# Kernel optimization log

Measured on AMD Instinct MI355X. Metric: run time of the kernel, lower is better.

Reference implementation:

```python
import jax, jax.numpy as jnp
import numpy as np

N = 50000   # nodes
E = 300000  # directed edges
IN = 512
H = 256
OUT = 256
K = 4096    # K_target; since K < N, pooled node count Kc == K statically


def setup_inputs() -> dict:
    key = jax.random.key(0)
    ks = jax.random.split(key, 8)
    x = jax.random.normal(ks[0], (N, IN), jnp.float32)
    edge_index = jax.random.randint(ks[1], (2, E), 0, N)
    W1 = jax.random.normal(ks[2], (IN, H), jnp.float32) / np.float32(np.sqrt(IN))
    b1 = jnp.zeros((H,), jnp.float32)
    W2 = jax.random.normal(ks[3], (H, OUT), jnp.float32) / np.float32(np.sqrt(H))
    b2 = jnp.zeros((OUT,), jnp.float32)
    w_score = jax.random.normal(ks[4], (H,), jnp.float32) / np.float32(np.sqrt(H))
    W_skip = jax.random.normal(ks[5], (H, OUT), jnp.float32) / np.float32(np.sqrt(H))
    b_skip = jnp.zeros((OUT,), jnp.float32)
    return dict(x=x, edge_index=edge_index, W1=W1, b1=b1, W2=W2, b2=b2,
                w_score=w_score, W_skip=W_skip, b_skip=b_skip)


def _gcn_sparse(x, src, dst, W, b, n):
    # PyG GCNConv(add_self_loops=True, normalize=True): out = D^{-1/2}(A+I)D^{-1/2} x W + b,
    # degrees computed on dst after adding self loops.
    h = x @ W
    loop = jnp.arange(n)
    s = jnp.concatenate([src, loop])
    d = jnp.concatenate([dst, loop])
    deg = jax.ops.segment_sum(jnp.ones_like(d, h.dtype), d, num_segments=n)
    dinv = jnp.where(deg > 0, jax.lax.rsqrt(deg), 0.0)
    coef = (dinv[s] * dinv[d])[:, None]
    return jax.ops.segment_sum(h[s] * coef, d, num_segments=n) + b


def _forward(x, edge_index, W1, b1, W2, b2, w_score, W_skip, b_skip):
    n = x.shape[0]
    src, dst = edge_index[0], edge_index[1]

    # conv1 + relu (dropout is identity in eval mode)
    x1 = jax.nn.relu(_gcn_sparse(x, src, dst, W1, b1, n))
    raw = x1 @ w_score                       # [N] score (Linear, no bias)
    x1g = x1 * jnp.tanh(raw)[:, None]        # gated features

    # top-K node selection
    _, kept = jax.lax.top_k(raw, K)          # sorted descending, like torch.topk
    keep_mask = jnp.zeros((n,), bool).at[kept].set(True)
    deg = jax.ops.segment_sum(jnp.ones((src.shape[0],), jnp.int32), src, num_segments=n)

    # cluster ids: kept nodes get 0..K-1 in topk order
    cid = jnp.full((n,), -1, jnp.int32).at[kept].set(jnp.arange(K, dtype=jnp.int32))

    # non-kept nodes join the kept (undirected) neighbor with max degree;
    # encode (degree, -node_id) so segment_max picks max degree, tie-break smallest id
    s_all = jnp.concatenate([src, dst])
    t_all = jnp.concatenate([dst, src])
    cand = jnp.where(keep_mask[t_all], deg[t_all] * n + (n - 1 - t_all), -1)
    best = jax.ops.segment_max(cand, s_all, num_segments=n)  # empty segs -> int min
    has = best >= 0
    best_t = (n - 1) - jnp.where(has, best % n, 0)
    # global fallback: kept node with max degree (tie-break: earliest in topk order)
    enc_k = deg[kept] * K + (K - 1 - jnp.arange(K))
    bg = kept[jnp.argmax(enc_k)]
    cid = jnp.where(keep_mask, cid, jnp.where(has, cid[best_t], cid[bg]))

    # mean pooling per cluster (pool_by_partition)
    sums = jax.ops.segment_sum(x1g, cid, num_segments=K)
    cnt = jnp.maximum(jax.ops.segment_sum(jnp.ones((n,), x.dtype), cid, num_segments=K), 1.0)
    xp = sums / cnt[:, None]

    # pooled edges with dedup + self-pair removal, as dense KxK adjacency (rows = dst)
    cu, cv = cid[src], cid[dst]
    A = jnp.zeros((K, K), x.dtype).at[cv, cu].max((cu != cv).astype(x.dtype))
    Ahat = A + jnp.eye(K, dtype=x.dtype)
    di = jax.lax.rsqrt(Ahat.sum(axis=1))     # deg >= 1 from self loops
    An = di[:, None] * Ahat * di[None, :]

    # conv2 on pooled graph, broadcast back, skip connection
    xp2 = An @ (xp @ W2) + b2
    return xp2[cid] + x1 @ W_skip + b_skip


def reference(x, edge_index, W1, b1, W2, b2, w_score, W_skip, b_skip):
    return _forward(x, edge_index, W1, b1, W2, b2, w_score, W_skip, b_skip)
```

## Files before the change

### kernel.cpp

```cpp
#include <hip/hip_runtime.h>
#include <hip/hip_bf16.h>

#define N_NODES 50000
#define E_EDGES 300000
#define IN_F 512
#define H_F 256
#define OUT_F 256
#define K_CL 4096
#define KW (K_CL / 32)
#define PCH 128
#define THRESH 192
#define MAXH 1024
#define NSPL 32
#define NB2 ((N_NODES + 255) / 256)
#define KBW ((N_NODES + 63) / 64 + 8)

typedef short bh8 __attribute__((ext_vector_type(8)));
typedef float f4 __attribute__((ext_vector_type(4)));
typedef unsigned short u16;
typedef unsigned long long u64;

__device__ __forceinline__ unsigned fkey(float f) {
    unsigned u = __float_as_uint(f);
    return (u & 0x80000000u) ? ~u : (u | 0x80000000u);
}

__device__ __forceinline__ u16 f2bf(float f) {
    __hip_bfloat16 b = __float2bfloat16(f);
    return *reinterpret_cast<u16*>(&b);
}

__device__ __forceinline__ float bf2f(u16 u) {
    return __uint_as_float(((unsigned)u) << 16);
}

__device__ __forceinline__ int getbit(const u64* __restrict__ bits, int i) {
    return (int)((bits[i >> 6] >> (i & 63)) & 1ULL);
}

__global__ __launch_bounds__(256) void init_nodes(int* cntD, int* degS,
                                                  unsigned long long* best_enc,
                                                  int* bgnode, int* heavycnt,
                                                  unsigned long long* bestpack,
                                                  unsigned* selT, int* curk, int* hist4) {
    int i = blockIdx.x * blockDim.x + threadIdx.x;
    if (i < N_NODES) { cntD[i] = 0; degS[i] = 0; best_enc[i] = 0ULL; }
    if (i < 1024) hist4[i] = 0;
    if (i == 0) {
        *heavycnt = 0; *bgnode = 0x7FFFFFFF; *bestpack = 0ULL;
        *selT = 0u; *curk = K_CL;
    }
}

__global__ __launch_bounds__(256) void deg_edges(const int* __restrict__ src,
                                                 const int* __restrict__ dst,
                                                 int* cntD, int* degS) {
    int e = blockIdx.x * blockDim.x + threadIdx.x;
    if (e >= E_EDGES) return;
    atomicAdd(&cntD[dst[e]], 1);
    atomicAdd(&degS[src[e]], 1);
}

#define SBM 64
#define SBN 128
#define SBK 16
__global__ __launch_bounds__(256) void gemm_f32s(const float* __restrict__ A,
                                                 const float* __restrict__ B,
                                                 float* __restrict__ C,
                                                 int M, int Nc, int Kd) {
    __shared__ float As[2][SBM][SBK];
    __shared__ float Bs[2][SBK][SBN];
    int tid = threadIdx.x;
    int tx = tid & 15;
    int ty = tid >> 4;
    int lane = tid & 63;
    int wave = tid >> 6;
    int row0 = blockIdx.y * SBM, col0 = blockIdx.x * SBN;
    float acc[4][8] = {};

    int arow = wave * 16 + (lane >> 2);
    int acolf = ((((lane & 3) * 16) ^ (((lane >> 4) & 1) << 5)) >> 2);

    auto stage_B = [&](int k0, int bb) {
        #pragma unroll
        for (int u = 0; u < 2; ++u) {
            int chunk = wave * 2 + u;
            int krow = chunk * 2 + (lane >> 5);
            const float* gsrc = &B[(long)(k0 + krow) * Nc + col0 + (lane & 31) * 4];
            __builtin_amdgcn_global_load_lds(
                (const __attribute__((address_space(1))) void*)gsrc,
                (__attribute__((address_space(3))) void*)&Bs[bb][chunk * 2][0],
                16, 0, 0);
        }
    };
    auto stage_A = [&](int k0, int bb) {
        int gr = row0 + arow;
        if (gr > M - 1) gr = M - 1;
        const float* gsrc = &A[(long)gr * Kd + k0 + acolf];
        __builtin_amdgcn_global_load_lds(
            (const __attribute__((address_space(1))) void*)gsrc,
            (__attribute__((address_space(3))) void*)&As[bb][wave * 16][0],
            16, 0, 0);
    };
    auto compute = [&](int bb) {
        #pragma unroll
        for (int kq = 0; kq < 4; ++kq) {
            float4 af[4];
            #pragma unroll
            for (int i = 0; i < 4; ++i) {
                int row = ty * 4 + i;
                int cb = ((kq * 16 ^ (((row >> 2) & 1) << 5)) >> 2);
                af[i] = *(const float4*)&As[bb][row][cb];
            }
            #pragma unroll
            for (int kk = 0; kk < 4; ++kk) {
                int k = kq * 4 + kk;
                float4 b0 = *(const float4*)&Bs[bb][k][tx * 4];
                float4 b1 = *(const float4*)&Bs[bb][k][tx * 4 + 64];
                float bv[8] = {b0.x, b0.y, b0.z, b0.w, b1.x, b1.y, b1.z, b1.w};
                float av[4] = {af[0][kk], af[1][kk], af[2][kk], af[3][kk]};
                #pragma unroll
                for (int i = 0; i < 4; ++i)
                    #pragma unroll
                    for (int j = 0; j < 8; ++j)
                        acc[i][j] += av[i] * bv[j];
            }
        }
    };

    stage_B(0, 0);
    stage_A(0, 0);
    __syncthreads();
    int nt = Kd / SBK;
    for (int t = 0; t < nt; ++t) {
        int cb = t & 1;
        if (t + 1 < nt) {
            stage_B(SBK * (t + 1), cb ^ 1);
            stage_A(SBK * (t + 1), cb ^ 1);
        }
        compute(cb);
        __syncthreads();
    }

    #pragma unroll
    for (int i = 0; i < 4; ++i) {
        int gr = row0 + ty * 4 + i;
        if (gr >= M) continue;
        float4 o0 = {acc[i][0], acc[i][1], acc[i][2], acc[i][3]};
        float4 o1 = {acc[i][4], acc[i][5], acc[i][6], acc[i][7]};
        *(float4*)&C[(long)gr * Nc + col0 + tx * 4] = o0;
        *(float4*)&C[(long)gr * Nc + col0 + 64 + tx * 4] = o1;
    }
}

__global__ __launch_bounds__(256) void pack_W2(const float* __restrict__ Wa, u16* Bpa,
                                               const float* __restrict__ Wb, u16* Bpb) {
    int k = blockIdx.x & 255;
    const float* W = (blockIdx.x < 256) ? Wa : Wb;
    u16* Bp = (blockIdx.x < 256) ? Bpa : Bpb;
    int col = threadIdx.x;
    int kb = k >> 5, g = (k >> 3) & 3, j = k & 7;
    Bp[(((long)(kb * 4 + g) * 256) + col) * 8 + j] = f2bf(W[(long)k * 256 + col]);
}

__global__ __launch_bounds__(256) void gemm_mfma(const u16* __restrict__ Ab,
                                                 const float* __restrict__ Af32,
                                                 const int* __restrict__ cnt,
                                                 const u16* __restrict__ Bp,
                                                 float* __restrict__ C,
                                                 int M,
                                                 const int* __restrict__ cid,
                                                 const float* __restrict__ xp2,
                                                 const float* __restrict__ bskip) {
    int tid = threadIdx.x;
    int w = tid >> 6, l = tid & 63;
    int lo16 = l & 15, hi4 = l >> 4;
    int arow = blockIdx.x * 64 + w * 16 + lo16;
    f4 acc[16];
    #pragma unroll
    for (int n = 0; n < 16; ++n) acc[n] = (f4){0.f, 0.f, 0.f, 0.f};

    float s = 1.f;
    if (Af32 && arow < M) s = 1.f / fmaxf((float)cnt[arow], 1.f);

    #pragma unroll
    for (int kb = 0; kb < 8; ++kb) {
        bh8 a = {0, 0, 0, 0, 0, 0, 0, 0};
        if (arow < M) {
            if (Af32) {
                float4 v0 = *(const float4*)&Af32[(long)arow * 256 + kb * 32 + hi4 * 8];
                float4 v1 = *(const float4*)&Af32[(long)arow * 256 + kb * 32 + hi4 * 8 + 4];
                u16 tmp[8] = {f2bf(v0.x * s), f2bf(v0.y * s), f2bf(v0.z * s), f2bf(v0.w * s),
                              f2bf(v1.x * s), f2bf(v1.y * s), f2bf(v1.z * s), f2bf(v1.w * s)};
                a = *(const bh8*)tmp;
            } else {
                a = *(const bh8*)&Ab[(long)arow * 256 + kb * 32 + hi4 * 8];
            }
        }
        const u16* bbase = &Bp[(((long)(kb * 4 + hi4)) * 256 + lo16) * 8];
        #pragma unroll
        for (int n = 0; n < 16; ++n) {
            bh8 b = *(const bh8*)&bbase[(long)n * 128];
            acc[n] = __builtin_amdgcn_mfma_f32_16x16x32_bf16(a, b, acc[n], 0, 0, 0);
        }
    }

    int orow0 = blockIdx.x * 64 + w * 16 + hi4 * 4;
    #pragma unroll
    for (int r = 0; r < 4; ++r) {
        int gr = orow0 + r;
        if (gr >= M) continue;
        long rb = (long)gr * 256;
        const float* xrow = cid ? (xp2 + (long)cid[gr] * 256) : nullptr;
        #pragma unroll
        for (int n = 0; n < 16; ++n) {
            int gc = n * 16 + lo16;
            float v = acc[n][r];
            if (cid) v += xrow[gc] + bskip[gc];
            C[rb + gc] = v;
        }
    }
}

__global__ __launch_bounds__(256) void scan_l1(const int* __restrict__ cnt,
                                               int* bsum, int n, float* dinv) {
    __shared__ int s[256];
    int t = threadIdx.x;
    int i = blockIdx.x * 256 + t;
    int v = (i < n) ? cnt[i] : 0;
    if (dinv && i < n) dinv[i] = rsqrtf((float)v + 1.0f);
    s[t] = v;
    __syncthreads();
    for (int off = 128; off > 0; off >>= 1) {
        if (t < off) s[t] += s[t + off];
        __syncthreads();
    }
    if (t == 0) bsum[blockIdx.x] = s[0];
}

__global__ __launch_bounds__(256) void scan_l2(const int* __restrict__ bsum,
                                               int* bstart, int nb) {
    __shared__ int s[256];
    int t = threadIdx.x;
    int v = (t < nb) ? bsum[t] : 0;
    s[t] = v;
    __syncthreads();
    for (int off = 1; off < 256; off <<= 1) {
        int a = (t >= off) ? s[t - off] : 0;
        __syncthreads();
        s[t] += a;
        __syncthreads();
    }
    if (t < nb) bstart[t] = s[t] - v;
}

__global__ __launch_bounds__(256) void scan_l3(const int* __restrict__ cnt,
                                               const int* __restrict__ bstart,
                                               int* start, int* cur, int n) {
    __shared__ int s[256];
    int t = threadIdx.x;
    int i = blockIdx.x * 256 + t;
    int v = (i < n) ? cnt[i] : 0;
    s[t] = v;
    __syncthreads();
    for (int off = 1; off < 256; off <<= 1) {
        int a = (t >= off) ? s[t - off] : 0;
        __syncthreads();
        s[t] += a;
        __syncthreads();
    }
    int st = bstart[blockIdx.x] + s[t] - v;
    if (i < n) { start[i] = st; cur[i] = st; }
    if (i == n - 1) start[n] = st + v;
}

__global__ __launch_bounds__(256) void csr_scatter(const int* __restrict__ src,
                                                   const int* __restrict__ dst,
                                                   int* cur, int* csr) {
    int e = blockIdx.x * blockDim.x + threadIdx.x;
    if (e >= E_EDGES) return;
    int d = dst[e];
    int p = atomicAdd(&cur[d], 1);
    csr[p] = src[e];
}

__global__ __launch_bounds__(64) void agg_fused(const float* __restrict__ h,
                                                const float* __restrict__ dinv,
                                                const int* __restrict__ rowptr,
                                                const int* __restrict__ csr,
                                                const float* __restrict__ b1,
                                                const float* __restrict__ w_score,
                                                u16* __restrict__ x1b,
                                                float* __restrict__ raw) {
    int i = blockIdx.x;
    int l = threadIdx.x;
    float di_ = dinv[i];
    const float4* H4 = (const float4*)h;
    long q = (long)i * 64 + l;
    float4 a = H4[q];
    float sc = di_ * di_;
    a.x *= sc; a.y *= sc; a.z *= sc; a.w *= sc;
    int p0 = rowptr[i], p1 = rowptr[i + 1];
    int t = p0;
    for (; t + 1 < p1; t += 2) {
        int s0 = csr[t], s1 = csr[t + 1];
        float c0 = dinv[s0] * di_;
        float c1 = dinv[s1] * di_;
        float4 h0 = H4[(long)s0 * 64 + l];
        float4 h1 = H4[(long)s1 * 64 + l];
        a.x += c0 * h0.x; a.y += c0 * h0.y; a.z += c0 * h0.z; a.w += c0 * h0.w;
        a.x += c1 * h1.x; a.y += c1 * h1.y; a.z += c1 * h1.z; a.w += c1 * h1.w;
    }
    if (t < p1) {
        int s0 = csr[t];
        float c0 = dinv[s0] * di_;
        float4 h0 = H4[(long)s0 * 64 + l];
        a.x += c0 * h0.x; a.y += c0 * h0.y; a.z += c0 * h0.z; a.w += c0 * h0.w;
    }
    float4 bb = ((const float4*)b1)[l];
    float v0 = fmaxf(a.x + bb.x, 0.f);
    float v1 = fmaxf(a.y + bb.y, 0.f);
    float v2 = fmaxf(a.z + bb.z, 0.f);
    float v3 = fmaxf(a.w + bb.w, 0.f);
    ushort4 o;
    o.x = f2bf(v0); o.y = f2bf(v1); o.z = f2bf(v2); o.w = f2bf(v3);
    ((ushort4*)x1b)[q] = o;
    float4 wv = ((const float4*)w_score)[l];
    float s2 = (v0 * wv.x + v2 * wv.z) + (v1 * wv.y + v3 * wv.w);
    #pragma unroll
    for (int off = 32; off > 0; off >>= 1)
        s2 += __shfl_xor(s2, off, 64);
    if (l == 0) raw[i] = s2;
}

__global__ __launch_bounds__(256) void radix_hist(const float* __restrict__ raw,
                                                  const unsigned* __restrict__ pPrefix,
                                                  int byte, int* hist) {
    __shared__ int lh[256];
    int t = threadIdx.x;
    lh[t] = 0;
    __syncthreads();
    int i = blockIdx.x * 256 + t;
    if (i < N_NODES) {
        unsigned key = fkey(raw[i]);
        unsigned known_mask = (byte == 3) ? 0u : (0xFFFFFFFFu << ((byte + 1) * 8));
        if ((key & known_mask) == *pPrefix)
            atomicAdd(&lh[(key >> (byte * 8)) & 255], 1);
    }
    __syncthreads();
    int hh = lh[t];
    if (hh) atomicAdd(&hist[t], hh);
}

__global__ __launch_bounds__(64) void radix_pick(const int* __restrict__ hist,
                                                 unsigned* pPrefix, int* pK, int byte) {
    if (threadIdx.x != 0) return;
    int kk = *pK;
    int cum = 0;
    int v = 255;
    for (; v > 0; --v) {
        int c = hist[v];
        if (cum + c >= kk) break;
        cum += c;
    }
    *pPrefix |= ((unsigned)v) << (byte * 8);
    *pK = kk - cum;
}

__global__ __launch_bounds__(256) void topk_count(const float* __restrict__ raw,
                                                  const unsigned* pT,
                                                  int* bGt, int* bEq) {
    __shared__ int sg[256], se[256];
    unsigned T = *pT;
    int t = threadIdx.x;
    int i = blockIdx.x * 256 + t;
    int gt = 0, eq = 0;
    if (i < N_NODES) {
        unsigned k = fkey(raw[i]);
        gt = k > T; eq = (k == T);
    }
    sg[t] = gt; se[t] = eq;
    __syncthreads();
    for (int off = 128; off > 0; off >>= 1) {
        if (t < off) { sg[t] += sg[t + off]; se[t] += se[t + off]; }
        __syncthreads();
    }
    if (t == 0) { bGt[blockIdx.x] = sg[0]; bEq[blockIdx.x] = se[0]; }
}

__global__ __launch_bounds__(256) void scan_blocks(const int* __restrict__ bGt,
                                                   const int* __restrict__ bEq,
                                                   int* gtStart, int* eqStart) {
    __shared__ int sg[256], se[256];
    int t = threadIdx.x;
    int vg = (t < NB2) ? bGt[t] : 0;
    int ve = (t < NB2) ? bEq[t] : 0;
    sg[t] = vg; se[t] = ve;
    __syncthreads();
    for (int off = 1; off < 256; off <<= 1) {
        int a = (t >= off) ? sg[t - off] : 0;
        int b = (t >= off) ? se[t - off] : 0;
        __syncthreads();
        sg[t] += a; se[t] += b;
        __syncthreads();
    }
    if (t < NB2) { gtStart[t] = sg[t] - vg; eqStart[t] = se[t] - ve; }
    if (t == 255) gtStart[NB2] = sg[255];
}

__global__ __launch_bounds__(256) void topk_assign(const float* __restrict__ raw,
                                                   const unsigned* pT, const int* pNeedEq,
                                                   const int* __restrict__ degS,
                                                   const int* __restrict__ gtStart,
                                                   const int* __restrict__ eqStart,
                                                   u64* keep_bits, int* cid,
                                                   unsigned long long* bestpack) {
    __shared__ int sg[256], se[256];
    unsigned T = *pT;
    int needEq = *pNeedEq;
    int totalGt = gtStart[NB2];
    int b = blockIdx.x, t = threadIdx.x;
    int i = b * 256 + t;
    int gt = 0, eq = 0;
    unsigned k = 0;
    if (i < N_NODES) {
        k = fkey(raw[i]);
        gt = k > T; eq = (k == T);
    }
    sg[t] = gt; se[t] = eq;
    __syncthreads();
    for (int off = 1; off < 256; off <<= 1) {
        int a = (t >= off) ? sg[t - off] : 0;
        int c = (t >= off) ? se[t - off] : 0;
        __syncthreads();
        sg[t] += a; se[t] += c;
        __syncthreads();
    }
    int eg = sg[t] - gt, ee = se[t] - eq;
    int kp = 0;
    unsigned long long p = 0ULL;
    if (i < N_NODES) {
        int c = -1;
        if (gt) { kp = 1; c = gtStart[b] + eg; }
        else if (eq) {
            int r = eqStart[b] + ee;
            if (r < needEq) { kp = 1; c = totalGt + r; }
        }
        cid[i] = c;
        if (kp) p = ((unsigned long long)(unsigned)degS[i] << 32) | k;
    }
    u64 ball = __ballot(kp);
    if ((t & 63) == 0) keep_bits[(b * 256 + t) >> 6] = ball;
    #pragma unroll
    for (int o = 32; o > 0; o >>= 1) {
        unsigned long long q = __shfl_xor((long long)p, o, 64);
        if (q > p) p = q;
    }
    if ((t & 63) == 0 && p) atomicMax(bestpack, p);
}

__global__ __launch_bounds__(256) void bg_node(const u64* __restrict__ keep_bits,
                                               const int* __restrict__ degS,
                                               const float* __restrict__ raw,
                                               const unsigned long long* bestpack, int* bgnode) {
    int i = blockIdx.x * blockDim.x + threadIdx.x;
    if (i < N_NODES && getbit(keep_bits, i)) {
        unsigned long long p = ((unsigned long long)(unsigned)degS[i] << 32) | fkey(raw[i]);
        if (p == *bestpack) atomicMin(bgnode, i);
    }
}

__global__ __launch_bounds__(256) void neigh_edges(const int* __restrict__ src,
                                                   const int* __restrict__ dst,
                                                   const u64* __restrict__ keep_bits,
                                                   const int* __restrict__ degS,
                                                   unsigned long long* best_enc) {
    int e = blockIdx.x * blockDim.x + threadIdx.x;
    if (e >= 2 * E_EDGES) return;
    int s, t;
    if (e < E_EDGES) { s = src[e]; t = dst[e]; }
    else { s = dst[e - E_EDGES]; t = src[e - E_EDGES]; }
    if (!getbit(keep_bits, s) && getbit(keep_bits, t)) {
        unsigned long long enc =
            (unsigned long long)((long long)degS[t] * N_NODES + (N_NODES - 1 - t)) + 1ULL;
        atomicMax(&best_enc[s], enc);
    }
}

__global__ __launch_bounds__(256) void resolve_cid(const u64* __restrict__ keep_bits,
                                                   const unsigned long long* __restrict__ best_enc,
                                                   const int* __restrict__ bgnode, int* cid) {
    int i = blockIdx.x * blockDim.x + threadIdx.x;
    if (i >= N_NODES) return;
    if (getbit(keep_bits, i)) return;
    unsigned long long v = best_enc[i];
    if (v > 0ULL) {
        long long enc = (long long)(v - 1ULL);
        int t = (N_NODES - 1) - (int)(enc % N_NODES);
        cid[i] = cid[t];
    } else {
        cid[i] = cid[*bgnode];
    }
}

#define NPB 1024
__global__ __launch_bounds__(256) void ccount2(const int* __restrict__ cid, int* ccnt) {
    __shared__ int hist[K_CL];
    for (int t = threadIdx.x; t < K_CL; t += 256) hist[t] = 0;
    __syncthreads();
    int base = blockIdx.x * NPB;
    #pragma unroll
    for (int u = 0; u < NPB / 256; ++u) {
        int idx = base + u * 256 + threadIdx.x;
        if (idx < N_NODES) atomicAdd(&hist[cid[idx]], 1);
    }
    __syncthreads();
    for (int t = threadIdx.x; t < K_CL; t += 256) {
        int hh = hist[t];
        if (hh) atomicAdd(&ccnt[t], hh);
    }
}

__global__ __launch_bounds__(256) void cscatter2(const int* __restrict__ cid,
                                                 int* ccur, int* clist) {
    __shared__ int hist[K_CL];
    for (int t = threadIdx.x; t < K_CL; t += 256) hist[t] = 0;
    __syncthreads();
    int base = blockIdx.x * NPB;
    int myc[NPB / 256], myr[NPB / 256];
    #pragma unroll
    for (int u = 0; u < NPB / 256; ++u) {
        int idx = base + u * 256 + threadIdx.x;
        if (idx < N_NODES) { myc[u] = cid[idx]; myr[u] = atomicAdd(&hist[myc[u]], 1); }
        else myc[u] = -1;
    }
    __syncthreads();
    for (int t = threadIdx.x; t < K_CL; t += 256) {
        int hh = hist[t];
        if (hh) hist[t] = atomicAdd(&ccur[t], hh);
    }
    __syncthreads();
    #pragma unroll
    for (int u = 0; u < NPB / 256; ++u)
        if (myc[u] >= 0) clist[hist[myc[u]] + myr[u]] = base + u * 256 + threadIdx.x;
}

__global__ __launch_bounds__(256) void pool_chunk(const u16* __restrict__ x1b,
                                                  const float* __restrict__ raw,
                                                  const int* __restrict__ clist,
                                                  const int* __restrict__ cid,
                                                  float* xp) {
    __shared__ int s_node[PCH];
    __shared__ int s_c[PCH];
    __shared__ float s_g[PCH];
    int j = threadIdx.x;
    int base = blockIdx.x * PCH;
    int m = N_NODES - base; if (m > PCH) m = PCH;
    for (int t = j; t < m; t += 256) {
        int nd = clist[base + t];
        s_node[t] = nd;
        s_c[t] = cid[nd];
        s_g[t] = tanhf(raw[nd]);
    }
    __syncthreads();
    float acc = 0.f;
    int cprev = s_c[0];
    for (int t = 0; t < m; t += 4) {
        int mm = m - t; if (mm > 4) mm = 4;
        float v[4];
        #pragma unroll
        for (int u = 0; u < 4; ++u)
            if (u < mm) v[u] = bf2f(x1b[(long)s_node[t + u] * H_F + j]);
        #pragma unroll
        for (int u = 0; u < 4; ++u) {
            if (u < mm) {
                int c = s_c[t + u];
                if (c != cprev) {
                    atomicAdd(&xp[(long)cprev * H_F + j], acc);
                    acc = 0.f;
                    cprev = c;
                }
                acc += s_g[t + u] * v[u];
            }
        }
    }
    atomicAdd(&xp[(long)cprev * H_F + j], acc);
}

__global__ __launch_bounds__(256) void build_Abits(const int* __restrict__ src,
                                                   const int* __restrict__ dst,
                                                   const int* __restrict__ cid,
                                                   unsigned* Abits) {
    int e = blockIdx.x * blockDim.x + threadIdx.x;
    if (e >= E_EDGES) return;
    int cu = cid[src[e]], cv = cid[dst[e]];
    if (cu != cv) atomicOr(&Abits[(long)cv * KW + (cu >> 5)], 1u << (cu & 31));
}

__global__ __launch_bounds__(256) void pop_di2(const unsigned* __restrict__ Abits, float* di,
                                               int* nnzA, int* heavy, int* heavycnt) {
    int i = blockIdx.x * blockDim.x + threadIdx.x;
    if (i >= K_CL) return;
    int c = 0;
    for (int w = 0; w < KW; ++w) c += __popc(Abits[(long)i * KW + w]);
    di[i] = rsqrtf((float)c + 1.0f);
    nnzA[i] = c;
    if (c > THRESH) {
        int p = atomicAdd(heavycnt, 1);
        if (p < MAXH) heavy[p] = i;
    }
}

__global__ __launch_bounds__(256) void spmm_light(const unsigned* __restrict__ Abits,
                                                  const float* __restrict__ xpW2,
                                                  const float* __restrict__ di,
                                                  const float* __restrict__ b2,
                                                  const int* __restrict__ nnzA,
                                                  float* xp2) {
    __shared__ unsigned s_row[KW];
    __shared__ float s_part[3][256];
    int cv = blockIdx.x;
    if (nnzA[cv] > THRESH) return;
    int tid = threadIdx.x;
    int w = tid >> 6, l = tid & 63;
    if (tid < KW) s_row[tid] = Abits[(long)cv * KW + tid];
    __syncthreads();
    float4 a0 = {0.f, 0.f, 0.f, 0.f}, a1 = {0.f, 0.f, 0.f, 0.f};
    const float4* Y4 = (const float4*)xpW2;
    for (int wi = w * 32; wi < w * 32 + 32; wi += 2) {
        unsigned w0 = s_row[wi], w1 = s_row[wi + 1];
        while (w0 | w1) {
            if (w0) {
                int b = __ffs(w0) - 1; w0 &= w0 - 1;
                int cu = wi * 32 + b;
                float d = di[cu];
                float4 y = Y4[(long)cu * 64 + l];
                a0.x += d * y.x; a0.y += d * y.y; a0.z += d * y.z; a0.w += d * y.w;
            }
            if (w1) {
                int b = __ffs(w1) - 1; w1 &= w1 - 1;
                int cu = (wi + 1) * 32 + b;
                float d = di[cu];
                float4 y = Y4[(long)cu * 64 + l];
                a1.x += d * y.x; a1.y += d * y.y; a1.z += d * y.z; a1.w += d * y.w;
            }
        }
    }
    float4 acc = {a0.x + a1.x, a0.y + a1.y, a0.z + a1.z, a0.w + a1.w};
    if (w > 0) *(float4*)&s_part[w - 1][l * 4] = acc;
    __syncthreads();
    if (w == 0) {
        #pragma unroll
        for (int ww = 0; ww < 3; ++ww) {
            float4 p = *(float4*)&s_part[ww][l * 4];
            acc.x += p.x; acc.y += p.y; acc.z += p.z; acc.w += p.w;
        }
        float dv = di[cv];
        float4 ys = Y4[(long)cv * 64 + l];
        float4 o;
        o.x = dv * (acc.x + dv * ys.x) + b2[l * 4 + 0];
        o.y = dv * (acc.y + dv * ys.y) + b2[l * 4 + 1];
        o.z = dv * (acc.z + dv * ys.z) + b2[l * 4 + 2];
        o.w = dv * (acc.w + dv * ys.w) + b2[l * 4 + 3];
        *(float4*)&xp2[(long)cv * H_F + l * 4] = o;
    }
}

__global__ __launch_bounds__(256) void spmm_heavy(const unsigned* __restrict__ Abits,
                                                  const float* __restrict__ xpW2,
                                                  const float* __restrict__ di,
                                                  const int* __restrict__ heavy,
                                                  const int* __restrict__ heavycnt,
                                                  float* Zacc) {
    __shared__ float s_part[3][256];
    int hi = blockIdx.x;
    int cnt = *heavycnt; if (cnt > MAXH) cnt = MAXH;
    if (hi >= cnt) return;
    int cv = heavy[hi];
    int sp = blockIdx.y;
    int tid = threadIdx.x;
    int w = tid >> 6, l = tid & 63;
    int wi = sp * (KW / NSPL) + w;
    unsigned word = Abits[(long)cv * KW + wi];
    float4 acc = {0.f, 0.f, 0.f, 0.f};
    const float4* Y4 = (const float4*)xpW2;
    while (word) {
        int b = __ffs(word) - 1; word &= word - 1;
        int cu = wi * 32 + b;
        float d = di[cu];
        float4 y = Y4[(long)cu * 64 + l];
        acc.x += d * y.x; acc.y += d * y.y; acc.z += d * y.z; acc.w += d * y.w;
    }
    if (w > 0) *(float4*)&s_part[w - 1][l * 4] = acc;
    __syncthreads();
    if (w == 0) {
        #pragma unroll
        for (int ww = 0; ww < 3; ++ww) {
            float4 p = *(float4*)&s_part[ww][l * 4];
            acc.x += p.x; acc.y += p.y; acc.z += p.z; acc.w += p.w;
        }
        float* zp = &Zacc[(long)cv * H_F + l * 4];
        atomicAdd(zp + 0, acc.x);
        atomicAdd(zp + 1, acc.y);
        atomicAdd(zp + 2, acc.z);
        atomicAdd(zp + 3, acc.w);
    }
}

__global__ __launch_bounds__(256) void heavy_epi(const float* __restrict__ Zacc,
                                                 const float* __restrict__ xpW2,
                                                 const float* __restrict__ di,
                                                 const float* __restrict__ b2,
                                                 const int* __restrict__ heavy,
                                                 const int* __restrict__ heavycnt,
                                                 float* xp2) {
    int hi = blockIdx.x;
    int cnt = *heavycnt; if (cnt > MAXH) cnt = MAXH;
    if (hi >= cnt) return;
    int cv = heavy[hi];
    int j = threadIdx.x;
    float dv = di[cv];
    xp2[(long)cv * H_F + j] =
        dv * (Zacc[(long)cv * H_F + j] + dv * xpW2[(long)cv * H_F + j]) + b2[j];
}

static inline size_t align256(size_t x) { return (x + 255) & ~(size_t)255; }

extern "C" void kernel_launch(void* const* d_in, const int* in_sizes, int n_in,
                              void* d_out, int out_size, void* d_ws, size_t ws_size,
                              hipStream_t stream) {
    const float* x      = (const float*)d_in[0];
    const int*   eidx   = (const int*)d_in[1];
    const float* W1     = (const float*)d_in[2];
    const float* b1     = (const float*)d_in[3];
    const float* W2     = (const float*)d_in[4];
    const float* b2     = (const float*)d_in[5];
    const float* wscore = (const float*)d_in[6];
    const float* Wskip  = (const float*)d_in[7];
    const float* bskip  = (const float*)d_in[8];
    float* out = (float*)d_out;

    const int* src = eidx;
    const int* dst = eidx + E_EDGES;

    char* ws = (char*)d_ws;
    size_t off = 0;
    auto alloc = [&](size_t bytes) { char* p = ws + off; off += align256(bytes); return p; };

    float* h     = (float*)alloc((size_t)N_NODES * H_F * 4);
    u16*   x1b   = (u16*)alloc((size_t)N_NODES * H_F * 2);
    float* raw   = (float*)alloc((size_t)N_NODES * 4);
    float* dinv  = (float*)alloc((size_t)N_NODES * 4);
    int*   cntD  = (int*)alloc((size_t)N_NODES * 4);
    int*   degS  = (int*)alloc((size_t)N_NODES * 4);
    u64*   keep_bits = (u64*)alloc((size_t)KBW * 8);
    int*   cid   = (int*)alloc((size_t)N_NODES * 4);
    unsigned long long* best_enc = (unsigned long long*)alloc((size_t)N_NODES * 8);
    int*   rowptr= (int*)alloc((size_t)(N_NODES + 1) * 4);
    int*   cur   = (int*)alloc((size_t)N_NODES * 4);
    int*   csr   = (int*)alloc((size_t)E_EDGES * 4);
    int*   ccnt  = (int*)alloc((size_t)K_CL * 4);
    int*   cstart= (int*)alloc((size_t)(K_CL + 1) * 4);
    int*   ccur  = (int*)alloc((size_t)K_CL * 4);
    int*   clist = (int*)alloc((size_t)N_NODES * 4);
    int*   bGt   = (int*)alloc((size_t)NB2 * 4);
    int*   bEq   = (int*)alloc((size_t)NB2 * 4);
    int*   gtStart = (int*)alloc((size_t)(NB2 + 1) * 4);
    int*   eqStart = (int*)alloc((size_t)NB2 * 4);
    int*   bsum  = (int*)alloc((size_t)256 * 4);
    int*   bstart= (int*)alloc((size_t)256 * 4);
    int*   hist4 = (int*)alloc((size_t)4 * 256 * 4);
    char*  small = alloc(64);
    unsigned* selT = (unsigned*)(small + 0);
    int* needEq    = (int*)(small + 4);
    int* bgnode    = (int*)(small + 8);
    int* heavycnt  = (int*)(small + 12);
    unsigned long long* bestpack = (unsigned long long*)(small + 16);
    float* xp    = (float*)alloc((size_t)K_CL * H_F * 4);
    unsigned* Abits = (unsigned*)alloc((size_t)K_CL * KW * 4);
    float* Zacc  = (float*)alloc((size_t)K_CL * H_F * 4);
    float* di    = (float*)alloc((size_t)K_CL * 4);
    int*   nnzA  = (int*)alloc((size_t)K_CL * 4);
    int*   heavy = (int*)alloc((size_t)MAXH * 4);
    float* xpW2  = (float*)alloc((size_t)K_CL * H_F * 4);
    float* xp2   = (float*)alloc((size_t)K_CL * H_F * 4);
    u16*  BpS   = (u16*)alloc((size_t)H_F * OUT_F * 2);
    u16*  Bp2   = (u16*)alloc((size_t)H_F * H_F * 2);
    (void)ws_size; (void)n_in; (void)in_sizes; (void)out_size;

    int nb = NB2;
    int eb = (E_EDGES + 255) / 256;

    init_nodes<<<nb, 256, 0, stream>>>(cntD, degS, best_enc, bgnode, heavycnt, bestpack,
                                       selT, needEq, hist4);
    deg_edges<<<eb, 256, 0, stream>>>(src, dst, cntD, degS);

    pack_W2<<<512, 256, 0, stream>>>(Wskip, BpS, W2, Bp2);

    {
        dim3 grid(H_F / SBN, (N_NODES + SBM - 1) / SBM);
        gemm_f32s<<<grid, 256, 0, stream>>>(x, W1, h, N_NODES, H_F, IN_F);
    }

    scan_l1<<<NB2, 256, 0, stream>>>(cntD, bsum, N_NODES, dinv);
    scan_l2<<<1, 256, 0, stream>>>(bsum, bstart, NB2);
    scan_l3<<<NB2, 256, 0, stream>>>(cntD, bstart, rowptr, cur, N_NODES);
    csr_scatter<<<eb, 256, 0, stream>>>(src, dst, cur, csr);
    agg_fused<<<N_NODES, 64, 0, stream>>>(h, dinv, rowptr, csr, b1, wscore, x1b, raw);

    for (int b = 3; b >= 0; --b) {
        radix_hist<<<NB2, 256, 0, stream>>>(raw, selT, b, hist4 + b * 256);
        radix_pick<<<1, 64, 0, stream>>>(hist4 + b * 256, selT, needEq, b);
    }
    topk_count<<<NB2, 256, 0, stream>>>(raw, selT, bGt, bEq);
    scan_blocks<<<1, 256, 0, stream>>>(bGt, bEq, gtStart, eqStart);
    topk_assign<<<NB2, 256, 0, stream>>>(raw, selT, needEq, degS, gtStart, eqStart,
                                         keep_bits, cid, bestpack);
    bg_node<<<nb, 256, 0, stream>>>(keep_bits, degS, raw, bestpack, bgnode);

    neigh_edges<<<(2 * E_EDGES + 255) / 256, 256, 0, stream>>>(src, dst, keep_bits, degS,
                                                               best_enc);
    resolve_cid<<<nb, 256, 0, stream>>>(keep_bits, best_enc, bgnode, cid);

    hipMemsetAsync(xp, 0, (size_t)K_CL * H_F * 4 * 2 + (size_t)K_CL * KW * 4, stream);

    hipMemsetAsync(ccnt, 0, (size_t)K_CL * 4, stream);
    {
        int cb = (N_NODES + NPB - 1) / NPB;
        ccount2<<<cb, 256, 0, stream>>>(cid, ccnt);
        scan_l1<<<K_CL / 256, 256, 0, stream>>>(ccnt, bsum, K_CL, nullptr);
        scan_l2<<<1, 256, 0, stream>>>(bsum, bstart, K_CL / 256);
        scan_l3<<<K_CL / 256, 256, 0, stream>>>(ccnt, bstart, cstart, ccur, K_CL);
        cscatter2<<<cb, 256, 0, stream>>>(cid, ccur, clist);
    }
    pool_chunk<<<(N_NODES + PCH - 1) / PCH, 256, 0, stream>>>(x1b, raw, clist, cid, xp);

    gemm_mfma<<<K_CL / 64, 256, 0, stream>>>(nullptr, xp, ccnt, Bp2, xpW2, K_CL,
                                             nullptr, nullptr, nullptr);

    build_Abits<<<eb, 256, 0, stream>>>(src, dst, cid, Abits);
    pop_di2<<<(K_CL + 255) / 256, 256, 0, stream>>>(Abits, di, nnzA, heavy, heavycnt);
    spmm_light<<<K_CL, 256, 0, stream>>>(Abits, xpW2, di, b2, nnzA, xp2);
    {
        dim3 hgrid(MAXH, NSPL);
        spmm_heavy<<<hgrid, 256, 0, stream>>>(Abits, xpW2, di, heavy, heavycnt, Zacc);
    }
    heavy_epi<<<MAXH, 256, 0, stream>>>(Zacc, xpW2, di, b2, heavy, heavycnt, xp2);

    gemm_mfma<<<(N_NODES + 63) / 64, 256, 0, stream>>>(x1b, nullptr, nullptr, BpS, out,
                                                       N_NODES, cid, xp2, bskip);
}
```

Baseline: 657.4 us.

## Fuse small post-topk kernels and drop heavy-row epilogue and Zacc buffer

Folds bg_node into the neighbour-edge kernel, merges resolve_cid with the cluster-count histogram, moves the ccnt zeroing into init_nodes, and removes the heavy_epi pass. spmm_light now writes the diagonal and bias term for heavy rows, and spmm_heavy atomically adds its scaled partial sums straight into xp2. This removes several launches, one memset and the Zacc buffer. The cost is a smaller block per histogram in the merged count kernel, which means more global atomics, and a new ordering dependency: spmm_heavy must run after spmm_light has initialised the heavy rows.

```diff
diff --git a/kernel.cpp b/kernel.cpp
--- a/kernel.cpp
+++ b/kernel.cpp
@@ -42,10 +42,12 @@
                                                   unsigned long long* best_enc,
                                                   int* bgnode, int* heavycnt,
                                                   unsigned long long* bestpack,
-                                                  unsigned* selT, int* curk, int* hist4) {
+                                                  unsigned* selT, int* curk,
+                                                  int* hist4, int* ccnt) {
     int i = blockIdx.x * blockDim.x + threadIdx.x;
     if (i < N_NODES) { cntD[i] = 0; degS[i] = 0; best_enc[i] = 0ULL; }
     if (i < 1024) hist4[i] = 0;
+    if (i < K_CL) ccnt[i] = 0;
     if (i == 0) {
         *heavycnt = 0; *bgnode = 0x7FFFFFFF; *bestpack = 0ULL;
         *selT = 0u; *curk = K_CL;
@@ -459,23 +461,19 @@
     if ((t & 63) == 0 && p) atomicMax(bestpack, p);
 }
 
-__global__ __launch_bounds__(256) void bg_node(const u64* __restrict__ keep_bits,
-                                               const int* __restrict__ degS,
-                                               const float* __restrict__ raw,
-                                               const unsigned long long* bestpack, int* bgnode) {
-    int i = blockIdx.x * blockDim.x + threadIdx.x;
-    if (i < N_NODES && getbit(keep_bits, i)) {
-        unsigned long long p = ((unsigned long long)(unsigned)degS[i] << 32) | fkey(raw[i]);
-        if (p == *bestpack) atomicMin(bgnode, i);
-    }
-}
-
-__global__ __launch_bounds__(256) void neigh_edges(const int* __restrict__ src,
-                                                   const int* __restrict__ dst,
-                                                   const u64* __restrict__ keep_bits,
-                                                   const int* __restrict__ degS,
-                                                   unsigned long long* best_enc) {
+__global__ __launch_bounds__(256) void neigh_bg(const int* __restrict__ src,
+                                                const int* __restrict__ dst,
+                                                const u64* __restrict__ keep_bits,
+                                                const int* __restrict__ degS,
+                                                const float* __restrict__ raw,
+                                                const unsigned long long* __restrict__ bestpack,
+                                                int* bgnode,
+                                                unsigned long long* best_enc) {
     int e = blockIdx.x * blockDim.x + threadIdx.x;
+    if (e < N_NODES && getbit(keep_bits, e)) {
+        unsigned long long p = ((unsigned long long)(unsigned)degS[e] << 32) | fkey(raw[e]);
+        if (p == *bestpack) atomicMin(bgnode, e);
+    }
     if (e >= 2 * E_EDGES) return;
     int s, t;
     if (e < E_EDGES) { s = src[e]; t = dst[e]; }
@@ -487,40 +485,40 @@
     }
 }
 
-__global__ __launch_bounds__(256) void resolve_cid(const u64* __restrict__ keep_bits,
-                                                   const unsigned long long* __restrict__ best_enc,
-                                                   const int* __restrict__ bgnode, int* cid) {
-    int i = blockIdx.x * blockDim.x + threadIdx.x;
-    if (i >= N_NODES) return;
-    if (getbit(keep_bits, i)) return;
-    unsigned long long v = best_enc[i];
-    if (v > 0ULL) {
-        long long enc = (long long)(v - 1ULL);
-        int t = (N_NODES - 1) - (int)(enc % N_NODES);
-        cid[i] = cid[t];
-    } else {
-        cid[i] = cid[*bgnode];
-    }
-}
-
-#define NPB 1024
-__global__ __launch_bounds__(256) void ccount2(const int* __restrict__ cid, int* ccnt) {
+__global__ __launch_bounds__(256) void resolve_cid_count(const u64* __restrict__ keep_bits,
+                                                         const unsigned long long* __restrict__ best_enc,
+                                                         const int* __restrict__ bgnode,
+                                                         int* cid, int* ccnt) {
     __shared__ int hist[K_CL];
-    for (int t = threadIdx.x; t < K_CL; t += 256) hist[t] = 0;
-    __syncthreads();
-    int base = blockIdx.x * NPB;
-    #pragma unroll
-    for (int u = 0; u < NPB / 256; ++u) {
-        int idx = base + u * 256 + threadIdx.x;
-        if (idx < N_NODES) atomicAdd(&hist[cid[idx]], 1);
-    }
-    __syncthreads();
-    for (int t = threadIdx.x; t < K_CL; t += 256) {
+    int tid = threadIdx.x;
+    for (int t = tid; t < K_CL; t += 256) hist[t] = 0;
+    __syncthreads();
+    int i = blockIdx.x * 256 + tid;
+    if (i < N_NODES) {
+        int c;
+        if (getbit(keep_bits, i)) {
+            c = cid[i];
+        } else {
+            unsigned long long v = best_enc[i];
+            if (v > 0ULL) {
+                long long enc = (long long)(v - 1ULL);
+                int t = (N_NODES - 1) - (int)(enc % N_NODES);
+                c = cid[t];
+            } else {
+                c = cid[*bgnode];
+            }
+            cid[i] = c;
+        }
+        atomicAdd(&hist[c], 1);
+    }
+    __syncthreads();
+    for (int t = tid; t < K_CL; t += 256) {
         int hh = hist[t];
         if (hh) atomicAdd(&ccnt[t], hh);
     }
 }
 
+#define NPB 1024
 __global__ __launch_bounds__(256) void cscatter2(const int* __restrict__ cid,
                                                  int* ccur, int* clist) {
     __shared__ int hist[K_CL];
@@ -620,8 +618,13 @@
     __shared__ unsigned s_row[KW];
     __shared__ float s_part[3][256];
     int cv = blockIdx.x;
-    if (nnzA[cv] > THRESH) return;
     int tid = threadIdx.x;
+    if (nnzA[cv] > THRESH) {
+        float dv = di[cv];
+        xp2[(long)cv * H_F + tid] =
+            dv * dv * xpW2[(long)cv * H_F + tid] + b2[tid];
+        return;
+    }
     int w = tid >> 6, l = tid & 63;
     if (tid < KW) s_row[tid] = Abits[(long)cv * KW + tid];
     __syncthreads();
@@ -671,7 +674,7 @@
                                                   const float* __restrict__ di,
                                                   const int* __restrict__ heavy,
                                                   const int* __restrict__ heavycnt,
-                                                  float* Zacc) {
+                                                  float* xp2) {
     __shared__ float s_part[3][256];
     int hi = blockIdx.x;
     int cnt = *heavycnt; if (cnt > MAXH) cnt = MAXH;
@@ -699,29 +702,13 @@
             float4 p = *(float4*)&s_part[ww][l * 4];
             acc.x += p.x; acc.y += p.y; acc.z += p.z; acc.w += p.w;
         }
-        float* zp = &Zacc[(long)cv * H_F + l * 4];
-        atomicAdd(zp + 0, acc.x);
-        atomicAdd(zp + 1, acc.y);
-        atomicAdd(zp + 2, acc.z);
-        atomicAdd(zp + 3, acc.w);
-    }
-}
-
-__global__ __launch_bounds__(256) void heavy_epi(const float* __restrict__ Zacc,
-                                                 const float* __restrict__ xpW2,
-                                                 const float* __restrict__ di,
-                                                 const float* __restrict__ b2,
-                                                 const int* __restrict__ heavy,
-                                                 const int* __restrict__ heavycnt,
-                                                 float* xp2) {
-    int hi = blockIdx.x;
-    int cnt = *heavycnt; if (cnt > MAXH) cnt = MAXH;
-    if (hi >= cnt) return;
-    int cv = heavy[hi];
-    int j = threadIdx.x;
-    float dv = di[cv];
-    xp2[(long)cv * H_F + j] =
-        dv * (Zacc[(long)cv * H_F + j] + dv * xpW2[(long)cv * H_F + j]) + b2[j];
+        float dv = di[cv];
+        float* zp = &xp2[(long)cv * H_F + l * 4];
+        atomicAdd(zp + 0, dv * acc.x);
+        atomicAdd(zp + 1, dv * acc.y);
+        atomicAdd(zp + 2, dv * acc.z);
+        atomicAdd(zp + 3, dv * acc.w);
+    }
 }
 
 static inline size_t align256(size_t x) { return (x + 255) & ~(size_t)255; }
@@ -778,7 +765,6 @@
     unsigned long long* bestpack = (unsigned long long*)(small + 16);
     float* xp    = (float*)alloc((size_t)K_CL * H_F * 4);
     unsigned* Abits = (unsigned*)alloc((size_t)K_CL * KW * 4);
-    float* Zacc  = (float*)alloc((size_t)K_CL * H_F * 4);
     float* di    = (float*)alloc((size_t)K_CL * 4);
     int*   nnzA  = (int*)alloc((size_t)K_CL * 4);
     int*   heavy = (int*)alloc((size_t)MAXH * 4);
@@ -788,11 +774,10 @@
     u16*  Bp2   = (u16*)alloc((size_t)H_F * H_F * 2);
     (void)ws_size; (void)n_in; (void)in_sizes; (void)out_size;
 
-    int nb = NB2;
     int eb = (E_EDGES + 255) / 256;
 
-    init_nodes<<<nb, 256, 0, stream>>>(cntD, degS, best_enc, bgnode, heavycnt, bestpack,
-                                       selT, needEq, hist4);
+    init_nodes<<<NB2, 256, 0, stream>>>(cntD, degS, best_enc, bgnode, heavycnt, bestpack,
+                                        selT, needEq, hist4, ccnt);
     deg_edges<<<eb, 256, 0, stream>>>(src, dst, cntD, degS);
 
     pack_W2<<<512, 256, 0, stream>>>(Wskip, BpS, W2, Bp2);
@@ -816,18 +801,15 @@
     scan_blocks<<<1, 256, 0, stream>>>(bGt, bEq, gtStart, eqStart);
     topk_assign<<<NB2, 256, 0, stream>>>(raw, selT, needEq, degS, gtStart, eqStart,
                                          keep_bits, cid, bestpack);
-    bg_node<<<nb, 256, 0, stream>>>(keep_bits, degS, raw, bestpack, bgnode);
-
-    neigh_edges<<<(2 * E_EDGES + 255) / 256, 256, 0, stream>>>(src, dst, keep_bits, degS,
-                                                               best_enc);
-    resolve_cid<<<nb, 256, 0, stream>>>(keep_bits, best_enc, bgnode, cid);
-
-    hipMemsetAsync(xp, 0, (size_t)K_CL * H_F * 4 * 2 + (size_t)K_CL * KW * 4, stream);
-
-    hipMemsetAsync(ccnt, 0, (size_t)K_CL * 4, stream);
+
+    neigh_bg<<<(2 * E_EDGES + 255) / 256, 256, 0, stream>>>(src, dst, keep_bits, degS,
+                                                            raw, bestpack, bgnode, best_enc);
+    resolve_cid_count<<<NB2, 256, 0, stream>>>(keep_bits, best_enc, bgnode, cid, ccnt);
+
+    hipMemsetAsync(xp, 0, (size_t)K_CL * H_F * 4 + (size_t)K_CL * KW * 4, stream);
+
     {
         int cb = (N_NODES + NPB - 1) / NPB;
-        ccount2<<<cb, 256, 0, stream>>>(cid, ccnt);
         scan_l1<<<K_CL / 256, 256, 0, stream>>>(ccnt, bsum, K_CL, nullptr);
         scan_l2<<<1, 256, 0, stream>>>(bsum, bstart, K_CL / 256);
         scan_l3<<<K_CL / 256, 256, 0, stream>>>(ccnt, bstart, cstart, ccur, K_CL);
@@ -843,9 +825,8 @@
     spmm_light<<<K_CL, 256, 0, stream>>>(Abits, xpW2, di, b2, nnzA, xp2);
     {
         dim3 hgrid(MAXH, NSPL);
-        spmm_heavy<<<hgrid, 256, 0, stream>>>(Abits, xpW2, di, heavy, heavycnt, Zacc);
-    }
-    heavy_epi<<<MAXH, 256, 0, stream>>>(Zacc, xpW2, di, b2, heavy, heavycnt, xp2);
+        spmm_heavy<<<hgrid, 256, 0, stream>>>(Abits, xpW2, di, heavy, heavycnt, xp2);
+    }
 
     gemm_mfma<<<(N_NODES + 63) / 64, 256, 0, stream>>>(x1b, nullptr, nullptr, BpS, out,
                                                        N_NODES, cid, xp2, bskip);
```

Result: no change. 654.3 us (-0.5%).
